# Optimization experiments

Measured on AMD Instinct MI355X. Metric: run time of the kernel, lower is better.

## Reference

```python
import jax, jax.numpy as jnp
import numpy as np

N, C, S = 64, 128, 12          # batch, channels, input_size
HW = S * S                      # 144
RIN = S ** 4


def setup_inputs() -> dict:
    key = jax.random.key(0)
    ks = jax.random.split(key, 6)
    x1 = jax.random.normal(ks[0], (N, C, S, S), dtype=jnp.float32)
    x2 = jax.random.normal(ks[1], (N, C, S, S), dtype=jnp.float32)
    # Linear weights stored [in, out]; scaled ~1/sqrt(fan_in) like torch default
    w1 = jax.random.normal(ks[2], (RIN, RIN // 4), dtype=jnp.float32) / np.sqrt(RIN)
    w2 = jax.random.normal(ks[3], (RIN // 4, RIN // 16), dtype=jnp.float32) / np.sqrt(RIN // 4)
    w3 = jax.random.normal(ks[4], (RIN // 16, RIN // 64), dtype=jnp.float32) / np.sqrt(RIN // 16)
    w4 = jax.random.normal(ks[5], (RIN // 64, 8), dtype=jnp.float32) / np.sqrt(RIN // 64)
    return {
        "x1": x1, "x2": x2,
        "w1": w1, "b1": jnp.zeros((RIN // 4,), jnp.float32),
        "w2": w2, "b2": jnp.zeros((RIN // 16,), jnp.float32),
        "w3": w3, "b3": jnp.zeros((RIN // 64,), jnp.float32),
        "w4": w4, "b4": jnp.zeros((8,), jnp.float32),
    }


def _l2_normalize(x):
    # torch: norm over dim=1 (channels), broadcast divide -> per-(n,h,w) unit vectors
    return x / jnp.linalg.norm(x, axis=1, keepdims=True)


def reference(x1, x2, w1, b1, w2, b2, w3, b3, w4, b4):
    n, c, h, w = x1.shape
    x1n = _l2_normalize(x1)
    x2n = _l2_normalize(x2)
    # out[n, k, i, j] = sum_c x1n[n,c,i,j] * x2n_flat[n,c,k]  (k flattens x2's HxW)
    corr = jnp.einsum('ncij,nck->nkij', x1n, x2n.reshape(n, c, h * w))  # [N, HW, H, W]
    x = corr.reshape(n, h * w * h * w)  # [N, S^4]
    x = jax.nn.relu(x @ w1 + b1)
    x = jax.nn.relu(x @ w2 + b2)
    x = jnp.tanh(x @ w3 + b3)
    H = x @ w4 + b4  # [N, 8]
    ones = jnp.ones((n, 1), dtype=H.dtype)
    return jnp.concatenate([H, ones], axis=1).reshape(n, 3, 3)
```

## Files before the change

### kernel.cpp

```cpp
#include <hip/hip_runtime.h>
#include <stdint.h>
#include <math.h>


typedef short short8 __attribute__((ext_vector_type(8)));
typedef float f32x4 __attribute__((ext_vector_type(4)));
typedef unsigned int uint2v __attribute__((ext_vector_type(2)));

__device__ __forceinline__ unsigned bf16u(float x) {
    return (__float_as_uint(x) + 0x8000u) >> 16;
}
__device__ __forceinline__ unsigned packbf(float a, float b) {
    return ((__float_as_uint(a) + 0x8000u) >> 16) |
           ((__float_as_uint(b) + 0x8000u) & 0xFFFF0000u);
}
__device__ __forceinline__ float bf2f(unsigned short u) {
    return __uint_as_float(((unsigned)u) << 16);
}

__global__ __launch_bounds__(256) void knorm(const float* __restrict__ x1,
                                             const float* __restrict__ x2,
                                             unsigned short* __restrict__ x1nt,
                                             unsigned short* __restrict__ x2nt) {
    __shared__ unsigned short s[128 * 148];
    __shared__ float rn[144];
    int b = blockIdx.x;
    int n = b >> 1;
    const float* src = (b & 1) ? x2 + n * 18432 : x1 + n * 18432;
    unsigned short* dst = (b & 1) ? x2nt + n * 18432 : x1nt + n * 18432;
    int t = threadIdx.x;
    for (int i = 0; i < 72; ++i) {
        int g = t + 256 * i;
        int c = g / 144, ij = g - c * 144;
        s[c * 148 + ij] = (unsigned short)bf16u(src[g]);
    }
    __syncthreads();
    if (t < 144) {
        float acc = 0.f;
        for (int c = 0; c < 128; ++c) {
            float v = bf2f(s[c * 148 + t]);
            acc += v * v;
        }
        rn[t] = 1.0f / sqrtf(acc);
    }
    __syncthreads();
    for (int i = 0; i < 72; ++i) {
        int o = t + 256 * i;
        int ij = o >> 7, c = o & 127;
        float v = bf2f(s[c * 148 + ij]);
        dst[o] = (unsigned short)bf16u(v * rn[ij]);
    }
}

__global__ __launch_bounds__(256) void kcorr(const unsigned short* __restrict__ x1nt,
                                             const unsigned short* __restrict__ x2nt,
                                             unsigned short* __restrict__ Abuf) {
    int n = blockIdx.x;
    int lane = threadIdx.x & 63;
    int w = threadIdx.x >> 6;
    int col = lane & 15, quad = lane >> 4;
    const unsigned short* p1 = x1nt + n * 18432;
    const unsigned short* p2 = x2nt + n * 18432;
    unsigned short* out = Abuf + n * 20736;
    for (int tt = w; tt < 81; tt += 4) {
        int m0 = (tt / 9) * 16, n0 = (tt % 9) * 16;
        f32x4 acc = {0.f, 0.f, 0.f, 0.f};
        const short8* a0 = (const short8*)(p2 + (m0 + col) * 128 + quad * 8);
        const short8* b0 = (const short8*)(p1 + (n0 + col) * 128 + quad * 8);
#pragma unroll
        for (int ks = 0; ks < 4; ++ks) {
            short8 a = a0[ks * 4];
            short8 bv = b0[ks * 4];
            acc = __builtin_amdgcn_mfma_f32_16x16x32_bf16(a, bv, acc, 0, 0, 0);
        }
#pragma unroll
        for (int r = 0; r < 4; ++r) {
            int row = m0 + quad * 4 + r;
            out[row * 144 + n0 + col] = (unsigned short)bf16u(acc[r]);
        }
    }
}

template <int N, int KTOT, int KCHUNK>
__global__ __launch_bounds__(256) void kgemm(const unsigned short* __restrict__ A,
                                             const float* __restrict__ W,
                                             float* __restrict__ Cf) {
    int lane = threadIdx.x & 63;
    int w = threadIdx.x >> 6;
    int col = lane & 15, quad = lane >> 4;
    int c0 = blockIdx.x * 64 + w * 16;
    if (c0 >= N) return;
    int kc = blockIdx.y * KCHUNK;
    const unsigned short* Ap = A + kc + quad * 8;
    const float* Wp = W + (size_t)(kc + quad * 8) * N + c0 + col;
    f32x4 acc0 = {0, 0, 0, 0}, acc1 = {0, 0, 0, 0}, acc2 = {0, 0, 0, 0}, acc3 = {0, 0, 0, 0};
#pragma unroll 2
    for (int ks = 0; ks < KCHUNK / 32; ++ks) {
        int kk = ks * 32;
        short8 a0 = *(const short8*)(Ap + (0 * 16 + col) * KTOT + kk);
        short8 a1 = *(const short8*)(Ap + (1 * 16 + col) * KTOT + kk);
        short8 a2 = *(const short8*)(Ap + (2 * 16 + col) * KTOT + kk);
        short8 a3 = *(const short8*)(Ap + (3 * 16 + col) * KTOT + kk);
        const float* wp = Wp + (size_t)kk * N;
        float b0 = __builtin_nontemporal_load(wp + 0 * (size_t)N);
        float b1 = __builtin_nontemporal_load(wp + 1 * (size_t)N);
        float b2 = __builtin_nontemporal_load(wp + 2 * (size_t)N);
        float b3 = __builtin_nontemporal_load(wp + 3 * (size_t)N);
        float b4 = __builtin_nontemporal_load(wp + 4 * (size_t)N);
        float b5 = __builtin_nontemporal_load(wp + 5 * (size_t)N);
        float b6 = __builtin_nontemporal_load(wp + 6 * (size_t)N);
        float b7 = __builtin_nontemporal_load(wp + 7 * (size_t)N);
        union { unsigned u[4]; short8 s; } bu;
        bu.u[0] = packbf(b0, b1);
        bu.u[1] = packbf(b2, b3);
        bu.u[2] = packbf(b4, b5);
        bu.u[3] = packbf(b6, b7);
        acc0 = __builtin_amdgcn_mfma_f32_16x16x32_bf16(a0, bu.s, acc0, 0, 0, 0);
        acc1 = __builtin_amdgcn_mfma_f32_16x16x32_bf16(a1, bu.s, acc1, 0, 0, 0);
        acc2 = __builtin_amdgcn_mfma_f32_16x16x32_bf16(a2, bu.s, acc2, 0, 0, 0);
        acc3 = __builtin_amdgcn_mfma_f32_16x16x32_bf16(a3, bu.s, acc3, 0, 0, 0);
    }
#pragma unroll
    for (int r = 0; r < 4; ++r) {
        int row0 = quad * 4 + r;
        atomicAdd(&Cf[(0 * 16 + row0) * N + c0 + col], acc0[r]);
        atomicAdd(&Cf[(1 * 16 + row0) * N + c0 + col], acc1[r]);
        atomicAdd(&Cf[(2 * 16 + row0) * N + c0 + col], acc2[r]);
        atomicAdd(&Cf[(3 * 16 + row0) * N + c0 + col], acc3[r]);
    }
}

template <int N>
__global__ __launch_bounds__(256) void kep(const float* __restrict__ Cf,
                                           const float* __restrict__ bias,
                                           unsigned short* __restrict__ Cb) {
    int idx = (blockIdx.x * 256 + threadIdx.x) * 4;
    int col = idx % N;
    f32x4 v = *(const f32x4*)(Cf + idx);
    f32x4 bb = *(const f32x4*)(bias + col);
    float r0 = fmaxf(v[0] + bb[0], 0.f);
    float r1 = fmaxf(v[1] + bb[1], 0.f);
    float r2 = fmaxf(v[2] + bb[2], 0.f);
    float r3 = fmaxf(v[3] + bb[3], 0.f);
    uint2v p = {packbf(r0, r1), packbf(r2, r3)};
    *(uint2v*)(Cb + idx) = p;
}

__global__ __launch_bounds__(384) void kgemm3(const unsigned short* __restrict__ C2b,
                                              const float* __restrict__ W3,
                                              float* __restrict__ C3f) {
    __shared__ float as[324];
    int n = blockIdx.x, sl = blockIdx.y;
    int t = threadIdx.x;
    if (t < 324) as[t] = bf2f(C2b[n * 1296 + sl * 324 + t]);
    __syncthreads();
    if (t < 324) {
        float acc = 0.f;
        const float* wp = W3 + sl * 324 * 324 + t;
#pragma unroll 4
        for (int k = 0; k < 324; ++k) acc += as[k] * wp[k * 324];
        atomicAdd(&C3f[n * 324 + t], acc);
    }
}

__global__ __launch_bounds__(384) void kep3g4(const float* __restrict__ C3f,
                                              const float* __restrict__ b3,
                                              const float* __restrict__ W4,
                                              const float* __restrict__ b4,
                                              float* __restrict__ out) {
    __shared__ float t3[324];
    int n = blockIdx.x, t = threadIdx.x;
    if (t < 324) t3[t] = tanhf(C3f[n * 324 + t] + b3[t]);
    __syncthreads();
    if (t < 8) {
        float acc = b4[t];
        for (int k = 0; k < 324; ++k) acc += t3[k] * W4[k * 8 + t];
        out[n * 9 + t] = acc;
    } else if (t == 8) {
        out[n * 9 + 8] = 1.0f;
    }
}

extern "C" void kernel_launch(void* const* d_in, const int* in_sizes, int n_in,
                              void* d_out, int out_size, void* d_ws, size_t ws_size,
                              hipStream_t stream) {
    const float* x1 = (const float*)d_in[0];
    const float* x2 = (const float*)d_in[1];
    const float* w1 = (const float*)d_in[2];
    const float* b1 = (const float*)d_in[3];
    const float* w2 = (const float*)d_in[4];
    const float* b2 = (const float*)d_in[5];
    const float* w3 = (const float*)d_in[6];
    const float* b3 = (const float*)d_in[7];
    const float* w4 = (const float*)d_in[8];
    const float* b4 = (const float*)d_in[9];
    float* out = (float*)d_out;

    char* ws = (char*)d_ws;
    unsigned short* x1nt = (unsigned short*)(ws + 0);
    unsigned short* x2nt = (unsigned short*)(ws + 2359296);
    unsigned short* Abuf = (unsigned short*)(ws + 4718592);
    float* C1f = (float*)(ws + 7372800);
    float* C2f = (float*)(ws + 8699904);
    float* C3f = (float*)(ws + 9031680);
    unsigned short* C1b = (unsigned short*)(ws + 9114624);
    unsigned short* C2b = (unsigned short*)(ws + 9778176);

    hipMemsetAsync(ws + 7372800, 0, 1741824, stream);
    knorm<<<128, 256, 0, stream>>>(x1, x2, x1nt, x2nt);
    kcorr<<<64, 256, 0, stream>>>(x1nt, x2nt, Abuf);
    kgemm<5184, 20736, 2592><<<dim3(81, 8), 256, 0, stream>>>(Abuf, w1, C1f);
    kep<5184><<<324, 256, 0, stream>>>(C1f, b1, C1b);
    kgemm<1296, 5184, 288><<<dim3(21, 18), 256, 0, stream>>>(C1b, w2, C2f);
    kep<1296><<<81, 256, 0, stream>>>(C2f, b2, C2b);
    kgemm3<<<dim3(64, 4), 384, 0, stream>>>(C2b, w3, C3f);
    kep3g4<<<64, 384, 0, stream>>>(C3f, b3, w4, b4, out);
}
```

Before: 794.1 us.

## Fuse normalization into correlation and bias+ReLU epilogues into next GEMMs

```diff
diff --git a/kernel.cpp b/kernel.cpp
--- a/kernel.cpp
+++ b/kernel.cpp
@@ -5,7 +5,6 @@
 
 typedef short short8 __attribute__((ext_vector_type(8)));
 typedef float f32x4 __attribute__((ext_vector_type(4)));
-typedef unsigned int uint2v __attribute__((ext_vector_type(2)));
 
 __device__ __forceinline__ unsigned bf16u(float x) {
     return (__float_as_uint(x) + 0x8000u) >> 16;
@@ -18,65 +17,53 @@
     return __uint_as_float(((unsigned)u) << 16);
 }
 
-__global__ __launch_bounds__(256) void knorm(const float* __restrict__ x1,
-                                             const float* __restrict__ x2,
-                                             unsigned short* __restrict__ x1nt,
-                                             unsigned short* __restrict__ x2nt) {
-    __shared__ unsigned short s[128 * 148];
-    __shared__ float rn[144];
-    int b = blockIdx.x;
-    int n = b >> 1;
-    const float* src = (b & 1) ? x2 + n * 18432 : x1 + n * 18432;
-    unsigned short* dst = (b & 1) ? x2nt + n * 18432 : x1nt + n * 18432;
-    int t = threadIdx.x;
-    for (int i = 0; i < 72; ++i) {
-        int g = t + 256 * i;
+__global__ __launch_bounds__(1024) void kcorr2(const float* __restrict__ x1,
+                                               const float* __restrict__ x2,
+                                               unsigned short* __restrict__ Abuf) {
+    __shared__ unsigned short s1[144 * 136];
+    __shared__ unsigned short s2[144 * 136];
+    __shared__ float rn1[144], rn2[144];
+    int n = blockIdx.x, t = threadIdx.x;
+    const float* p1 = x1 + n * 18432;
+    const float* p2 = x2 + n * 18432;
+#pragma unroll
+    for (int i = 0; i < 18; ++i) {
+        int g = t + 1024 * i;
         int c = g / 144, ij = g - c * 144;
-        s[c * 148 + ij] = (unsigned short)bf16u(src[g]);
+        s1[ij * 136 + c] = (unsigned short)bf16u(p1[g]);
+        s2[ij * 136 + c] = (unsigned short)bf16u(p2[g]);
     }
     __syncthreads();
     if (t < 144) {
         float acc = 0.f;
-        for (int c = 0; c < 128; ++c) {
-            float v = bf2f(s[c * 148 + t]);
-            acc += v * v;
-        }
-        rn[t] = 1.0f / sqrtf(acc);
-    }
-    __syncthreads();
-    for (int i = 0; i < 72; ++i) {
-        int o = t + 256 * i;
-        int ij = o >> 7, c = o & 127;
-        float v = bf2f(s[c * 148 + ij]);
-        dst[o] = (unsigned short)bf16u(v * rn[ij]);
-    }
-}
-
-__global__ __launch_bounds__(256) void kcorr(const unsigned short* __restrict__ x1nt,
-                                             const unsigned short* __restrict__ x2nt,
-                                             unsigned short* __restrict__ Abuf) {
-    int n = blockIdx.x;
-    int lane = threadIdx.x & 63;
-    int w = threadIdx.x >> 6;
+        for (int c = 0; c < 128; ++c) { float v = bf2f(s1[t * 136 + c]); acc += v * v; }
+        rn1[t] = 1.0f / sqrtf(acc);
+    } else if (t < 288) {
+        int ij = t - 144;
+        float acc = 0.f;
+        for (int c = 0; c < 128; ++c) { float v = bf2f(s2[ij * 136 + c]); acc += v * v; }
+        rn2[ij] = 1.0f / sqrtf(acc);
+    }
+    __syncthreads();
+    int lane = t & 63, w = t >> 6;
     int col = lane & 15, quad = lane >> 4;
-    const unsigned short* p1 = x1nt + n * 18432;
-    const unsigned short* p2 = x2nt + n * 18432;
     unsigned short* out = Abuf + n * 20736;
-    for (int tt = w; tt < 81; tt += 4) {
+    for (int tt = w; tt < 81; tt += 16) {
         int m0 = (tt / 9) * 16, n0 = (tt % 9) * 16;
         f32x4 acc = {0.f, 0.f, 0.f, 0.f};
-        const short8* a0 = (const short8*)(p2 + (m0 + col) * 128 + quad * 8);
-        const short8* b0 = (const short8*)(p1 + (n0 + col) * 128 + quad * 8);
+        const short8* a0 = (const short8*)(s2 + (m0 + col) * 136 + quad * 8);
+        const short8* b0 = (const short8*)(s1 + (n0 + col) * 136 + quad * 8);
 #pragma unroll
         for (int ks = 0; ks < 4; ++ks) {
             short8 a = a0[ks * 4];
             short8 bv = b0[ks * 4];
             acc = __builtin_amdgcn_mfma_f32_16x16x32_bf16(a, bv, acc, 0, 0, 0);
         }
+        float rc = rn1[n0 + col];
 #pragma unroll
         for (int r = 0; r < 4; ++r) {
             int row = m0 + quad * 4 + r;
-            out[row * 144 + n0 + col] = (unsigned short)bf16u(acc[r]);
+            out[row * 144 + n0 + col] = (unsigned short)bf16u(acc[r] * rn2[row] * rc);
         }
     }
 }
@@ -89,7 +76,6 @@
     int w = threadIdx.x >> 6;
     int col = lane & 15, quad = lane >> 4;
     int c0 = blockIdx.x * 64 + w * 16;
-    if (c0 >= N) return;
     int kc = blockIdx.y * KCHUNK;
     const unsigned short* Ap = A + kc + quad * 8;
     const float* Wp = W + (size_t)(kc + quad * 8) * N + c0 + col;
@@ -102,14 +88,14 @@
         short8 a2 = *(const short8*)(Ap + (2 * 16 + col) * KTOT + kk);
         short8 a3 = *(const short8*)(Ap + (3 * 16 + col) * KTOT + kk);
         const float* wp = Wp + (size_t)kk * N;
-        float b0 = __builtin_nontemporal_load(wp + 0 * (size_t)N);
-        float b1 = __builtin_nontemporal_load(wp + 1 * (size_t)N);
-        float b2 = __builtin_nontemporal_load(wp + 2 * (size_t)N);
-        float b3 = __builtin_nontemporal_load(wp + 3 * (size_t)N);
-        float b4 = __builtin_nontemporal_load(wp + 4 * (size_t)N);
-        float b5 = __builtin_nontemporal_load(wp + 5 * (size_t)N);
-        float b6 = __builtin_nontemporal_load(wp + 6 * (size_t)N);
-        float b7 = __builtin_nontemporal_load(wp + 7 * (size_t)N);
+        float b0 = wp[0 * (size_t)N];
+        float b1 = wp[1 * (size_t)N];
+        float b2 = wp[2 * (size_t)N];
+        float b3 = wp[3 * (size_t)N];
+        float b4 = wp[4 * (size_t)N];
+        float b5 = wp[5 * (size_t)N];
+        float b6 = wp[6 * (size_t)N];
+        float b7 = wp[7 * (size_t)N];
         union { unsigned u[4]; short8 s; } bu;
         bu.u[0] = packbf(b0, b1);
         bu.u[1] = packbf(b2, b3);
@@ -130,29 +116,76 @@
     }
 }
 
-template <int N>
-__global__ __launch_bounds__(256) void kep(const float* __restrict__ Cf,
-                                           const float* __restrict__ bias,
-                                           unsigned short* __restrict__ Cb) {
-    int idx = (blockIdx.x * 256 + threadIdx.x) * 4;
-    int col = idx % N;
-    f32x4 v = *(const f32x4*)(Cf + idx);
-    f32x4 bb = *(const f32x4*)(bias + col);
-    float r0 = fmaxf(v[0] + bb[0], 0.f);
-    float r1 = fmaxf(v[1] + bb[1], 0.f);
-    float r2 = fmaxf(v[2] + bb[2], 0.f);
-    float r3 = fmaxf(v[3] + bb[3], 0.f);
-    uint2v p = {packbf(r0, r1), packbf(r2, r3)};
-    *(uint2v*)(Cb + idx) = p;
-}
-
-__global__ __launch_bounds__(384) void kgemm3(const unsigned short* __restrict__ C2b,
+template <int N, int KTOT, int KCHUNK>
+__global__ __launch_bounds__(256) void kgemm2f(const float* __restrict__ Af,
+                                               const float* __restrict__ bias,
+                                               const float* __restrict__ W,
+                                               float* __restrict__ Cf) {
+    int lane = threadIdx.x & 63;
+    int w = threadIdx.x >> 6;
+    int col = lane & 15, quad = lane >> 4;
+    int c0 = blockIdx.x * 64 + w * 16;
+    if (c0 >= N) return;
+    int kc = blockIdx.y * KCHUNK;
+    int kb = kc + quad * 8;
+    const float* Ap = Af + kb;
+    const float* Wp = W + (size_t)kb * N + c0 + col;
+    f32x4 acc0 = {0, 0, 0, 0}, acc1 = {0, 0, 0, 0}, acc2 = {0, 0, 0, 0}, acc3 = {0, 0, 0, 0};
+#pragma unroll 2
+    for (int ks = 0; ks < KCHUNK / 32; ++ks) {
+        int kk = ks * 32;
+        f32x4 bb0 = *(const f32x4*)(bias + kb + kk);
+        f32x4 bb1 = *(const f32x4*)(bias + kb + kk + 4);
+        union { unsigned u[4]; short8 s; } au[4];
+#pragma unroll
+        for (int i = 0; i < 4; ++i) {
+            const float* ap = Ap + (size_t)(i * 16 + col) * KTOT + kk;
+            f32x4 v0 = *(const f32x4*)(ap);
+            f32x4 v1 = *(const f32x4*)(ap + 4);
+            float r0 = fmaxf(v0[0] + bb0[0], 0.f), r1 = fmaxf(v0[1] + bb0[1], 0.f);
+            float r2 = fmaxf(v0[2] + bb0[2], 0.f), r3 = fmaxf(v0[3] + bb0[3], 0.f);
+            float r4 = fmaxf(v1[0] + bb1[0], 0.f), r5 = fmaxf(v1[1] + bb1[1], 0.f);
+            float r6 = fmaxf(v1[2] + bb1[2], 0.f), r7 = fmaxf(v1[3] + bb1[3], 0.f);
+            au[i].u[0] = packbf(r0, r1); au[i].u[1] = packbf(r2, r3);
+            au[i].u[2] = packbf(r4, r5); au[i].u[3] = packbf(r6, r7);
+        }
+        const float* wp = Wp + (size_t)kk * N;
+        float b0 = wp[0 * (size_t)N];
+        float b1 = wp[1 * (size_t)N];
+        float b2 = wp[2 * (size_t)N];
+        float b3 = wp[3 * (size_t)N];
+        float b4 = wp[4 * (size_t)N];
+        float b5 = wp[5 * (size_t)N];
+        float b6 = wp[6 * (size_t)N];
+        float b7 = wp[7 * (size_t)N];
+        union { unsigned u[4]; short8 s; } bu;
+        bu.u[0] = packbf(b0, b1);
+        bu.u[1] = packbf(b2, b3);
+        bu.u[2] = packbf(b4, b5);
+        bu.u[3] = packbf(b6, b7);
+        acc0 = __builtin_amdgcn_mfma_f32_16x16x32_bf16(au[0].s, bu.s, acc0, 0, 0, 0);
+        acc1 = __builtin_amdgcn_mfma_f32_16x16x32_bf16(au[1].s, bu.s, acc1, 0, 0, 0);
+        acc2 = __builtin_amdgcn_mfma_f32_16x16x32_bf16(au[2].s, bu.s, acc2, 0, 0, 0);
+        acc3 = __builtin_amdgcn_mfma_f32_16x16x32_bf16(au[3].s, bu.s, acc3, 0, 0, 0);
+    }
+#pragma unroll
+    for (int r = 0; r < 4; ++r) {
+        int row0 = quad * 4 + r;
+        atomicAdd(&Cf[(0 * 16 + row0) * N + c0 + col], acc0[r]);
+        atomicAdd(&Cf[(1 * 16 + row0) * N + c0 + col], acc1[r]);
+        atomicAdd(&Cf[(2 * 16 + row0) * N + c0 + col], acc2[r]);
+        atomicAdd(&Cf[(3 * 16 + row0) * N + c0 + col], acc3[r]);
+    }
+}
+
+__global__ __launch_bounds__(384) void kgemm3(const float* __restrict__ C2f,
+                                              const float* __restrict__ b2,
                                               const float* __restrict__ W3,
                                               float* __restrict__ C3f) {
     __shared__ float as[324];
     int n = blockIdx.x, sl = blockIdx.y;
     int t = threadIdx.x;
-    if (t < 324) as[t] = bf2f(C2b[n * 1296 + sl * 324 + t]);
+    if (t < 324) as[t] = fmaxf(C2f[n * 1296 + sl * 324 + t] + b2[sl * 324 + t], 0.f);
     __syncthreads();
     if (t < 324) {
         float acc = 0.f;
@@ -197,22 +230,15 @@
     float* out = (float*)d_out;
 
     char* ws = (char*)d_ws;
-    unsigned short* x1nt = (unsigned short*)(ws + 0);
-    unsigned short* x2nt = (unsigned short*)(ws + 2359296);
-    unsigned short* Abuf = (unsigned short*)(ws + 4718592);
-    float* C1f = (float*)(ws + 7372800);
-    float* C2f = (float*)(ws + 8699904);
-    float* C3f = (float*)(ws + 9031680);
-    unsigned short* C1b = (unsigned short*)(ws + 9114624);
-    unsigned short* C2b = (unsigned short*)(ws + 9778176);
-
-    hipMemsetAsync(ws + 7372800, 0, 1741824, stream);
-    knorm<<<128, 256, 0, stream>>>(x1, x2, x1nt, x2nt);
-    kcorr<<<64, 256, 0, stream>>>(x1nt, x2nt, Abuf);
+    unsigned short* Abuf = (unsigned short*)(ws + 0);
+    float* C1f = (float*)(ws + 2654208);
+    float* C2f = (float*)(ws + 3981312);
+    float* C3f = (float*)(ws + 4313088);
+
+    hipMemsetAsync(ws + 2654208, 0, 1741824, stream);
+    kcorr2<<<64, 1024, 0, stream>>>(x1, x2, Abuf);
     kgemm<5184, 20736, 2592><<<dim3(81, 8), 256, 0, stream>>>(Abuf, w1, C1f);
-    kep<5184><<<324, 256, 0, stream>>>(C1f, b1, C1b);
-    kgemm<1296, 5184, 288><<<dim3(21, 18), 256, 0, stream>>>(C1b, w2, C2f);
-    kep<1296><<<81, 256, 0, stream>>>(C2f, b2, C2b);
-    kgemm3<<<dim3(64, 4), 384, 0, stream>>>(C2b, w3, C3f);
+    kgemm2f<1296, 5184, 288><<<dim3(21, 18), 256, 0, stream>>>(C1f, b1, w2, C2f);
+    kgemm3<<<dim3(64, 4), 384, 0, stream>>>(C2f, b2, w3, C3f);
     kep3g4<<<64, 384, 0, stream>>>(C3f, b3, w4, b4, out);
 }
```

Result: faster. 750.5 us (-5.5%).
